# Kernel optimization log

Measured on AMD Instinct MI355X. Metric: run time of the kernel, lower is better.

The kernel has to match this reference:

```python
import jax, jax.numpy as jnp
import numpy as np

B, T = 1024, 39
NUM_C, NUM_STU, NUM_E, EMB = 123, 100000, 50000, 256
H = 123
IN1 = NUM_C + EMB  # 379


def setup_inputs() -> dict:
    key = jax.random.key(0)
    ks = jax.random.split(key, 32)
    f = lambda k, shp, s: jax.random.normal(k, shp, dtype=jnp.float32) * s
    inp = {}
    inp["q_maritx"] = jax.random.uniform(ks[0], (B, T, NUM_C), dtype=jnp.float32)
    inp["q_maritx_next"] = jax.random.uniform(ks[1], (B, T, NUM_C), dtype=jnp.float32)
    inp["concept"] = jax.random.randint(ks[2], (B, T), 0, NUM_C + 1)
    inp["s_id"] = jax.random.randint(ks[3], (B, 1), 0, NUM_STU + 1)
    inp["e_id"] = jax.random.randint(ks[4], (B, T), 0, NUM_E + 1)
    inp["r"] = jax.random.randint(ks[5], (B, T), 0, 2)
    inp["q_next"] = jax.random.randint(ks[6], (B, T), 0, NUM_E + 1)
    inp["concept_next"] = jax.random.randint(ks[7], (B, T), 0, NUM_C + 1)
    # learned parameters
    inp["emb_problem"] = f(ks[8], (NUM_E + 1, EMB), 1.0)
    inp["student_W"] = f(ks[9], (NUM_STU + 1, NUM_C), 1.0)
    inp["k_diff_W"] = f(ks[10], (NUM_E + 1, NUM_C), 1.0)
    inp["e_disc_W"] = f(ks[11], (NUM_E + 1, 1), 1.0)
    inp["answer_W"] = f(ks[12], (2, EMB), 1.0)
    inp["zz_W"] = f(ks[13], (NUM_C, NUM_C), 0.05)
    inp["zz_b"] = jnp.zeros((NUM_C,), jnp.float32)
    inp["d_t"] = f(ks[14], (1,), 1.0)
    inp["d_e"] = f(ks[15], (1,), 1.0)
    inp["W_ih"] = f(ks[16], (H, IN1), 0.05)
    inp["b_ih"] = jnp.zeros((H,), jnp.float32)
    inp["W_hh"] = f(ks[17], (H, H), 0.05)
    inp["b_hh"] = jnp.zeros((H,), jnp.float32)
    inp["W_tg"] = f(ks[18], (H, 1), 0.05)
    inp["b_tg"] = jnp.zeros((H,), jnp.float32)
    inp["W_z"] = f(ks[19], (H, IN1 + H), 0.05)
    inp["b_z"] = jnp.zeros((H,), jnp.float32)
    inp["W_h"] = f(ks[20], (H, IN1 + H), 0.05)
    inp["b_h"] = jnp.zeros((H,), jnp.float32)
    inp["p1_W"] = f(ks[21], (256, 502), 0.05)
    inp["p1_b"] = jnp.zeros((256,), jnp.float32)
    inp["p2_W"] = f(ks[22], (123, 256), 0.05)
    inp["p2_b"] = jnp.zeros((123,), jnp.float32)
    inp["p3_W"] = f(ks[23], (1, 123), 0.05)
    inp["p3_b"] = jnp.zeros((1,), jnp.float32)
    return inp


def _forward(q_maritx, q_maritx_next, emb_problem, student_W, k_diff_W, e_disc_W,
             answer_W, zz_W, zz_b, d_t, d_e, W_ih, b_ih, W_hh, b_hh, W_tg, b_tg,
             W_z, b_z, W_h, b_h, p1_W, p1_b, p2_W, p2_b, p3_W, p3_b,
             s_id, e_id, r, q_next):
    Bc, Tc = e_id.shape
    e_next_emb = emb_problem[q_next]                       # [B,T,256]
    s_prof = jax.nn.sigmoid(student_W[s_id])               # [B,1,123] (broadcasts vs repeat(1,39,1))
    k_diff = jax.nn.sigmoid(k_diff_W[e_id])                # [B,T,123]
    e_disc = jax.nn.sigmoid(e_disc_W[e_id]) * d_e          # [B,T,1]
    r_emb = answer_W[r]                                    # [B,T,256]
    concept_ab = jnp.einsum('btk,hk->bth', q_maritx, zz_W) + zz_b  # [B,T,123]
    x1 = jnp.concatenate([concept_ab * s_prof, r_emb], axis=-1)    # [B,T,379]
    # --- time-gated RNN: h_t = tanh(W_ih x_t + W_hh h + b) * sigmoid(tg(t)) ---
    Xp = jnp.einsum('bti,hi->bth', x1, W_ih) + b_ih
    tvec = jnp.arange(Tc, dtype=Xp.dtype)[:, None]
    gates = jax.nn.sigmoid(tvec * W_tg[:, 0][None, :] + b_tg)      # [T,123]
    h0 = jnp.zeros((Bc, W_hh.shape[0]), Xp.dtype)

    def step1(h, xs):
        xp, g = xs
        h = jnp.tanh(xp + h @ W_hh.T + b_hh) * g
        return h, h

    _, ys1 = jax.lax.scan(step1, h0, (Xp.transpose(1, 0, 2), gates))
    out_zz = ys1.transpose(1, 0, 2)                        # [B,T,123]
    # --- GRU-like cell (W_r unused in original forward) ---
    input_x1 = e_disc * (d_t * s_prof + (1.0 - d_t) * out_zz - k_diff) * q_maritx
    x2 = jnp.concatenate([input_x1, r_emb], axis=-1)       # [B,T,379]
    nin = x2.shape[-1]
    Wz_x, Wz_h = W_z[:, :nin], W_z[:, nin:]
    Wh_x, Wh_h = W_h[:, :nin], W_h[:, nin:]
    Zx = jnp.einsum('bti,hi->bth', x2, Wz_x) + b_z
    Hx = jnp.einsum('bti,hi->bth', x2, Wh_x) + b_h

    def step2(h, xs):
        zx, hx = xs
        z = jax.nn.sigmoid(zx + h @ Wz_h.T)
        ht = jnp.tanh(hx + h @ Wh_h.T)
        h = (1.0 - z) * h + z * ht
        return h, h

    _, ys2 = jax.lax.scan(step2, h0, (Zx.transpose(1, 0, 2), Hx.transpose(1, 0, 2)))
    outputs = ys2.transpose(1, 0, 2)                       # [B,T,123]
    hcat = jnp.concatenate([outputs, e_next_emb, q_maritx_next], axis=-1)  # [B,T,502]
    o1 = jax.nn.sigmoid(hcat @ p1_W.T + p1_b)  # dropout as identity (deterministic reference)
    o2 = jax.nn.sigmoid(o1 @ p2_W.T + p2_b)
    return jax.nn.sigmoid(o2 @ p3_W.T + p3_b)              # [B,T,1]


def reference(q_maritx, q_maritx_next, emb_problem, student_W, k_diff_W, e_disc_W,
              answer_W, zz_W, zz_b, d_t, d_e, W_ih, b_ih, W_hh, b_hh, W_tg, b_tg,
              W_z, b_z, W_h, b_h, p1_W, p1_b, p2_W, p2_b, p3_W, p3_b,
              concept, s_id, e_id, r, q_next, concept_next):
    # concept / concept_next embeddings are computed but unused in the original output
    return _forward(q_maritx, q_maritx_next, emb_problem, student_W, k_diff_W,
                    e_disc_W, answer_W, zz_W, zz_b, d_t, d_e, W_ih, b_ih, W_hh,
                    b_hh, W_tg, b_tg, W_z, b_z, W_h, b_h, p1_W, p1_b, p2_W,
                    p2_b, p3_W, p3_b, s_id, e_id, r, q_next)
```

## Files before the change

### kernel.cpp

```cpp
#include <hip/hip_runtime.h>
#include <hip/hip_bf16.h>

#define NRB 39936
#define BB 1024
#define TT 39
#define CC 123
#define EMBD 256
#define PCH 136

typedef __attribute__((ext_vector_type(8))) short short8;
typedef __attribute__((ext_vector_type(4))) short shortv4;
typedef __attribute__((ext_vector_type(4))) float floatx4;
typedef unsigned short us;

__device__ __forceinline__ float rcp_(float x){ return __builtin_amdgcn_rcpf(x); }
__device__ __forceinline__ float fsig(float x){ return rcp_(1.f + __expf(-x)); }
__device__ __forceinline__ float ftanh(float x){
  float ax = __builtin_fabsf(x);
  float e = __expf(-2.f*ax);
  float r = (1.f - e) * rcp_(1.f + e);
  return __builtin_copysignf(r, x);
}
__device__ __forceinline__ us f2bf(float x){
  union { float f; unsigned u; } v; v.f = x;
  unsigned r = v.u + 0x7FFFu + ((v.u >> 16) & 1u);
  return (us)(r >> 16);
}
__device__ __forceinline__ us f2bfh(float x){
  __bf16 h = (__bf16)x;
  return __builtin_bit_cast(us, h);
}
__device__ __forceinline__ float bf2f(us u){
  union { unsigned u; float f; } v; v.u = ((unsigned)u) << 16; return v.f;
}

__device__ __forceinline__ void lds_barrier(){
  __builtin_amdgcn_sched_barrier(0);
  asm volatile("s_waitcnt lgkmcnt(0)" ::: "memory");
  __builtin_amdgcn_s_barrier();
  __builtin_amdgcn_sched_barrier(0);
}

__device__ __forceinline__ void gl_lds16(void* lds, const void* g){
  __builtin_amdgcn_global_load_lds(
      (const __attribute__((address_space(1))) unsigned int*)g,
      (__attribute__((address_space(3))) unsigned int*)lds, 16, 0, 0);
}

#define G_RC 6
#define G_CW 1088
#define G_CAST 2496
#define G_HCAT 1872
#define G_PRE (G_RC + G_CW + G_CAST + G_HCAT)

__global__ __launch_bounds__(256) void k_pre(
    const float* __restrict__ W_ih, const float* __restrict__ W_z,
    const float* __restrict__ W_h, const float* __restrict__ answer_W,
    const float* __restrict__ zz_W, const float* __restrict__ W_hh,
    const float* __restrict__ p1_W, const float* __restrict__ p2_W,
    const float* __restrict__ emb, const int* __restrict__ q_next,
    const float* __restrict__ qmn, const float* __restrict__ q_m,
    float* __restrict__ rtab, us* __restrict__ wts,
    us* __restrict__ p1bf, us* __restrict__ p2bf,
    us* __restrict__ qbf, us* __restrict__ Abf)
{
  const int blk = blockIdx.x, tid = threadIdx.x;
  if (blk < G_RC){
    int which = blk >> 1, j = blk & 1, h = tid;
    if (h >= CC) return;
    const float* W; int stride;
    if (which==0){ W=W_ih; stride=379; } else if (which==1){ W=W_z; stride=502; } else { W=W_h; stride=502; }
    const float* a = answer_W + j*EMBD;
    const float* w = W + (size_t)h*stride + CC;
    float acc = 0.f;
    #pragma unroll 8
    for (int i=0;i<EMBD;i++) acc += w[i]*a[i];
    rtab[(which*2+j)*128 + h] = acc;
    return;
  }
  if (blk < G_RC + G_CW){
    int i = (blk - G_RC)*256 + tid;
    if (i < 7*16384){
      int w = i >> 14, idx = i & 16383, n = idx >> 7, k = idx & 127;
      float v = 0.f;
      if (n < CC && k < CC){
        if      (w==0) v = zz_W[n*CC + k];
        else if (w==1) v = W_ih[n*379 + k];
        else if (w==2) v = W_z [n*502 + k];
        else if (w==3) v = W_h [n*502 + k];
        else if (w==4) v = W_hh[n*CC + k];
        else if (w==5) v = W_z [n*502 + 379 + k];
        else           v = W_h [n*502 + 379 + k];
      }
      wts[i] = f2bf(v);
      return;
    }
    int j = i - 7*16384;
    if (j < 256*512){
      int n = j >> 9, k = j & 511;
      float v;
      if      (k < 379) v = p1_W[n*502 + k + 123];
      else if (k < 384) v = 0.f;
      else if (k < 507) v = p1_W[n*502 + (k - 384)];
      else              v = 0.f;
      p1bf[j] = f2bf(v);
      return;
    }
    j -= 256*512;
    if (j < 128*256){
      int n = j >> 8, k = j & 255;
      p2bf[j] = f2bf(n < CC ? p2_W[n*256 + k] : 0.f);
    }
    return;
  }
  if (blk < G_RC + G_CW + G_CAST){
    const size_t total = (size_t)NRB*128;
    for (size_t i = (size_t)(blk - G_RC - G_CW)*256 + tid; i < total; i += (size_t)G_CAST*256){
      int col = (int)(i & 127); size_t rp = i >> 7;
      int t = (int)(rp >> 10), b = (int)(rp & 1023);
      float v = (col < CC) ? q_m[((size_t)b*TT + t)*CC + col] : 0.f;
      qbf[i] = f2bf(v);
    }
    return;
  }
  {
    const size_t nchunk = (size_t)NRB*48;
    for (size_t c = (size_t)(blk - G_RC - G_CW - G_CAST)*256 + tid; c < nchunk; c += (size_t)G_HCAT*256){
      size_t row = c / 48;
      int c0 = (int)(c - row*48) * 8;
      short8 o;
      if (c0 < 256){
        int qn = q_next[row];
        float4 v0 = *(const float4*)(emb + (size_t)qn*EMBD + c0);
        float4 v1 = *(const float4*)(emb + (size_t)qn*EMBD + c0 + 4);
        o[0]=f2bf(v0.x); o[1]=f2bf(v0.y); o[2]=f2bf(v0.z); o[3]=f2bf(v0.w);
        o[4]=f2bf(v1.x); o[5]=f2bf(v1.y); o[6]=f2bf(v1.z); o[7]=f2bf(v1.w);
      } else {
        int j0 = c0 - 256;
        #pragma unroll
        for (int jj=0;jj<8;jj++){
          int j = j0 + jj;
          o[jj] = (j < CC) ? f2bf(qmn[row*CC + j]) : (short)0;
        }
      }
      *(short8*)(Abf + row*512 + c0) = o;
    }
  }
}

__global__ __launch_bounds__(256) void k_zz_elem(
    const us* __restrict__ X, const us* __restrict__ W,
    const float* __restrict__ zz_b,
    const float* __restrict__ q_m, const int* __restrict__ s_id,
    const int* __restrict__ e_id, const float* __restrict__ student_W,
    const float* __restrict__ k_diff_W, const float* __restrict__ e_disc_W,
    const float* __restrict__ d_t_p, const float* __restrict__ d_e_p,
    us* __restrict__ x1a, us* __restrict__ pre2, us* __restrict__ cqb)
{
  __shared__ __align__(16) us Asl[16][64][8];
  const int tid = threadIdx.x, w = tid >> 6, l = tid & 63, q = l >> 4, r16 = l & 15;
  const int rTile = blockIdx.x*64;
  short8 bfr[2][4];
  #pragma unroll
  for (int nt=0;nt<2;nt++){
    int n = w*32 + nt*16 + r16;
    #pragma unroll
    for (int kt=0;kt<4;kt++)
      bfr[nt][kt] = *(const short8*)(W + (size_t)n*128 + kt*32 + q*8);
  }
  #pragma unroll
  for (int i=0;i<4;i++){
    int seg = i*4 + w;
    gl_lds16(&Asl[seg][l][0], X + (size_t)(rTile+l)*128 + seg*8);
  }
  floatx4 acc[4][2];
  #pragma unroll
  for (int mt=0;mt<4;mt++){
    #pragma unroll
    for (int nt=0;nt<2;nt++){ acc[mt][nt][0]=0.f; acc[mt][nt][1]=0.f; acc[mt][nt][2]=0.f; acc[mt][nt][3]=0.f; }
  }
  __syncthreads();
  #pragma unroll
  for (int kt=0;kt<4;kt++){
    short8 af[4];
    #pragma unroll
    for (int mt=0;mt<4;mt++) af[mt] = *(const short8*)&Asl[kt*4+q][mt*16+r16][0];
    #pragma unroll
    for (int mt=0;mt<4;mt++){
      #pragma unroll
      for (int nt=0;nt<2;nt++)
        acc[mt][nt] = __builtin_amdgcn_mfma_f32_16x16x32_bf16(af[mt], bfr[nt][kt], acc[mt][nt], 0,0,0);
    }
  }
  const float dt = d_t_p[0], de = d_e_p[0];
  float zzb[2]; int colv[2];
  #pragma unroll
  for (int nt=0;nt<2;nt++){
    int col = w*32 + nt*16 + r16; colv[nt] = col;
    zzb[nt] = (col < CC) ? zz_b[col] : 0.f;
  }
  const int t = rTile >> 10;
  #pragma unroll
  for (int mt=0;mt<4;mt++){
    #pragma unroll
    for (int i=0;i<4;i++){
      int row = rTile + mt*16 + q*4 + i;
      int b = row & 1023;
      int g = b*TT + t;
      int btile = b >> 4, r = b & 15;
      int sid = s_id[b];
      int e   = e_id[g];
      float ed = fsig(e_disc_W[e]) * de;
      size_t base = ((size_t)t*64 + btile)*2048;
      #pragma unroll
      for (int nt=0;nt<2;nt++){
        int col = colv[nt];
        float x1v = 0.f, p2v = 0.f, cqv = 0.f;
        if (col < CC){
          float ab = acc[mt][nt][i] + zzb[nt];
          float sp = fsig(student_W[(size_t)sid*CC + col]);
          float kd = fsig(k_diff_W[(size_t)e*CC + col]);
          float qv = q_m[(size_t)g*CC + col];
          x1v = ab*sp;
          p2v = ed*(dt*sp - kd)*qv;
          cqv = ed*(1.f - dt)*qv;
        }
        x1a[base + (size_t)(((col>>5)*64 + ((col>>3)&3)*16 + r)*8) + (col&7)] = f2bf(x1v);
        size_t off = base + (size_t)(((col>>5)*64 + ((r>>2))*16 + (col&15))*8) + ((col>>4)&1)*4 + (r&3);
        pre2[off] = f2bf(p2v);
        cqb[off]  = f2bf(cqv);
      }
    }
  }
}

__global__ __launch_bounds__(512,1) void k_mid(
    const us* __restrict__ x1a, const us* __restrict__ pre2, const us* __restrict__ cqb,
    const us* __restrict__ Wih, const us* __restrict__ Whh,
    const us* __restrict__ Wzx, const us* __restrict__ Whx,
    const us* __restrict__ Wzh, const us* __restrict__ Whh2,
    const float* __restrict__ b_ih, const float* __restrict__ b_z, const float* __restrict__ b_h,
    const float* __restrict__ W_tg, const float* __restrict__ b_tg,
    const float* __restrict__ rtab, const int* __restrict__ r_idx,
    us* __restrict__ Abf)
{
  __shared__ __align__(16) us h1s[2][16*PCH];
  __shared__ __align__(16) us x2s[2][16*PCH];
  __shared__ __align__(16) us h2s[2][16*PCH];
  __shared__ int rint[TT*16];
  const int tid = threadIdx.x, w = tid >> 6, l = tid & 63, q = l >> 4, r16 = l & 15;
  const int bbase = blockIdx.x*16;
  const int n = w*16 + r16;

  short8 fih[4], fhh[4], fzx[4], fhx[4], fzh[4], fh2w[4];
  #pragma unroll
  for (int kt=0;kt<4;kt++){
    size_t wofs = (size_t)n*128 + kt*32 + q*8;
    fih[kt]  = *(const short8*)(Wih  + wofs);
    fhh[kt]  = *(const short8*)(Whh  + wofs);
    fzx[kt]  = *(const short8*)(Wzx  + wofs);
    fhx[kt]  = *(const short8*)(Whx  + wofs);
    fzh[kt]  = *(const short8*)(Wzh  + wofs);
    fh2w[kt] = *(const short8*)(Whh2 + wofs);
  }
  const bool vc = n < CC;
  const float bih = vc? b_ih[n]:0.f, bzv = vc? b_z[n]:0.f, bhv = vc? b_h[n]:0.f;
  const float wg = vc? W_tg[n]:0.f, bg = vc? b_tg[n]:0.f;
  const float r10 = vc? rtab[n]:0.f,     r11 = vc? rtab[128+n]:0.f;
  const float r20 = vc? rtab[256+n]:0.f, r21 = vc? rtab[384+n]:0.f;
  const float r30 = vc? rtab[512+n]:0.f, r31 = vc? rtab[640+n]:0.f;

  for (int i = tid; i < TT*16; i += 512)
    rint[i] = r_idx[(size_t)(bbase + (i & 15))*TT + (i >> 4)];
  for (int i = tid; i < 16*PCH; i += 512){ h1s[1][i] = 0; h2s[1][i] = 0; }

  short8 x1c[4];
  shortv4 pc4, cc4;
  {
    size_t base = (size_t)blockIdx.x*2048;
    #pragma unroll
    for (int kt=0;kt<4;kt++)
      x1c[kt] = *(const short8*)(x1a + base + (size_t)(kt*64 + q*16 + r16)*8);
    size_t cofs = base + (size_t)((w>>1)*64 + q*16 + r16)*8 + (size_t)(w&1)*4;
    pc4 = *(const shortv4*)(pre2 + cofs);
    cc4 = *(const shortv4*)(cqb + cofs);
  }
  __syncthreads();

  floatx4 accx;
  #pragma unroll
  for (int i=0;i<4;i++){ int rs = rint[q*4 + i]; accx[i] = bih + (rs ? r11 : r10); }
  #pragma unroll
  for (int kt=0;kt<4;kt++)
    accx = __builtin_amdgcn_mfma_f32_16x16x32_bf16(x1c[kt], fih[kt], accx, 0,0,0);

  floatx4 hold; hold[0]=0.f; hold[1]=0.f; hold[2]=0.f; hold[3]=0.f;

  for (int t=0; t<TT; t++){
    const int pA = t & 1, pO = pA ^ 1;
    short8 x1n[4]; shortv4 pcn, ccn;
    if (t < TT-1){
      size_t base = ((size_t)(t+1)*64 + blockIdx.x)*2048;
      #pragma unroll
      for (int kt=0;kt<4;kt++)
        x1n[kt] = *(const short8*)(x1a + base + (size_t)(kt*64 + q*16 + r16)*8);
      size_t cofs = base + (size_t)((w>>1)*64 + q*16 + r16)*8 + (size_t)(w&1)*4;
      pcn = *(const shortv4*)(pre2 + cofs);
      ccn = *(const shortv4*)(cqb + cofs);
    }
    short8 fr1[4];
    #pragma unroll
    for (int kt=0;kt<4;kt++)
      fr1[kt] = *(const short8*)&h1s[pO][r16*PCH + kt*32 + q*8];
    floatx4 acc1 = accx;
    #pragma unroll
    for (int kt=0;kt<4;kt++)
      acc1 = __builtin_amdgcn_mfma_f32_16x16x32_bf16(fr1[kt], fhh[kt], acc1, 0,0,0);
    float g = fsig((float)t*wg + bg);
    #pragma unroll
    for (int i=0;i<4;i++){
      float h1v = ftanh(acc1[i]) * g;
      h1s[pA][(q*4+i)*PCH + n] = f2bfh(h1v);
      float xv = bf2f((us)pc4[i]) + bf2f((us)cc4[i])*h1v;
      x2s[pA][(q*4+i)*PCH + n] = f2bfh(xv);
    }
    lds_barrier();
    if (t >= 1 && tid < 256){
      int row = tid >> 4, cs = tid & 15;
      short8 hv8 = *(const short8*)&h2s[pO][row*PCH + cs*8];
      *(short8*)(Abf + ((size_t)(bbase + row)*TT + (t-1))*512 + 384 + cs*8) = hv8;
    }
    short8 fx[4], fh[4];
    #pragma unroll
    for (int kt=0;kt<4;kt++){
      fx[kt] = *(const short8*)&x2s[pA][r16*PCH + kt*32 + q*8];
      fh[kt] = *(const short8*)&h2s[pO][r16*PCH + kt*32 + q*8];
    }
    floatx4 az, ahh;
    #pragma unroll
    for (int i=0;i<4;i++){
      int rs = rint[t*16 + q*4 + i];
      az[i]  = bzv + (rs ? r21 : r20);
      ahh[i] = bhv + (rs ? r31 : r30);
    }
    #pragma unroll
    for (int kt=0;kt<4;kt++){
      az  = __builtin_amdgcn_mfma_f32_16x16x32_bf16(fx[kt], fzx[kt], az, 0,0,0);
      az  = __builtin_amdgcn_mfma_f32_16x16x32_bf16(fh[kt], fzh[kt], az, 0,0,0);
      ahh = __builtin_amdgcn_mfma_f32_16x16x32_bf16(fx[kt], fhx[kt], ahh, 0,0,0);
      ahh = __builtin_amdgcn_mfma_f32_16x16x32_bf16(fh[kt], fh2w[kt], ahh, 0,0,0);
    }
    #pragma unroll
    for (int i=0;i<4;i++){
      float z  = fsig(az[i]);
      float th = ftanh(ahh[i]);
      hold[i] += z*(th - hold[i]);
      h2s[pA][(q*4+i)*PCH + n] = f2bfh(hold[i]);
    }
    if (t < TT-1){
      #pragma unroll
      for (int i=0;i<4;i++){ int rs = rint[(t+1)*16 + q*4 + i]; accx[i] = bih + (rs ? r11 : r10); }
      #pragma unroll
      for (int kt=0;kt<4;kt++)
        accx = __builtin_amdgcn_mfma_f32_16x16x32_bf16(x1n[kt], fih[kt], accx, 0,0,0);
      pc4 = pcn; cc4 = ccn;
    }
  }
  __syncthreads();
  if (tid < 256){
    int row = tid >> 4, cs = tid & 15;
    short8 hv8 = *(const short8*)&h2s[(TT-1)&1][row*PCH + cs*8];
    *(short8*)(Abf + ((size_t)(bbase + row)*TT + (TT-1))*512 + 384 + cs*8) = hv8;
  }
}

__global__ __launch_bounds__(256) void k_out(
    const us* __restrict__ Abf, const us* __restrict__ p1bf,
    const float* __restrict__ p1_b, const us* __restrict__ p2bf,
    const float* __restrict__ p2_b, const float* __restrict__ p3_W,
    const float* __restrict__ p3_b, float* __restrict__ out)
{
  __shared__ __align__(16) us smem[20480];
  __shared__ float red[64][4];
  us* Asl = smem;
  us* Bsl = smem + 4096;
  us* o1s = smem;
  const int tid = threadIdx.x;
  const int w = tid >> 6, l = tid & 63;
  const int q = l >> 4, r16 = l & 15;
  const int rTile = blockIdx.x * 64;
  floatx4 acc[4][4];
  #pragma unroll
  for (int a=0;a<4;a++){
    #pragma unroll
    for (int b=0;b<4;b++){ acc[a][b][0]=0.f; acc[a][b][1]=0.f; acc[a][b][2]=0.f; acc[a][b][3]=0.f; }
  }
  for (int c = 0; c < 8; c++){
    const int k0 = c*64;
    #pragma unroll
    for (int i=0;i<2;i++){
      int u = i*256 + tid; int seg = u>>6, m = u&63;
      gl_lds16(&Asl[(seg*64 + m)*8], Abf + (size_t)(rTile+m)*512 + k0 + seg*8);
    }
    #pragma unroll
    for (int i=0;i<8;i++){
      int u = i*256 + tid; int seg = u>>8, nn = u&255;
      gl_lds16(&Bsl[(seg*256 + nn)*8], p1bf + (size_t)nn*512 + k0 + seg*8);
    }
    __syncthreads();
    #pragma unroll
    for (int ks=0; ks<2; ks++){
      int seg = ks*4 + q;
      short8 af[4], bfr[4];
      #pragma unroll
      for (int mt=0;mt<4;mt++) af[mt] = *(const short8*)&Asl[(seg*64 + mt*16 + r16)*8];
      #pragma unroll
      for (int nt=0;nt<4;nt++) bfr[nt] = *(const short8*)&Bsl[(seg*256 + w*64 + nt*16 + r16)*8];
      #pragma unroll
      for (int mt=0;mt<4;mt++){
        #pragma unroll
        for (int nt=0;nt<4;nt++)
          acc[mt][nt] = __builtin_amdgcn_mfma_f32_16x16x32_bf16(af[mt], bfr[nt], acc[mt][nt], 0,0,0);
      }
    }
    __syncthreads();
  }
  #pragma unroll
  for (int nt=0;nt<4;nt++){
    int col = w*64 + nt*16 + r16;
    float bb = p1_b[col];
    #pragma unroll
    for (int mt=0;mt<4;mt++){
      #pragma unroll
      for (int i=0;i<4;i++)
        o1s[(mt*16 + q*4 + i)*264 + col] = f2bf(fsig(acc[mt][nt][i] + bb));
    }
  }
  __syncthreads();
  short8 bf2[2][8];
  #pragma unroll
  for (int nt=0;nt<2;nt++){
    int n2 = w*32 + nt*16 + r16;
    #pragma unroll
    for (int kt=0;kt<8;kt++)
      bf2[nt][kt] = *(const short8*)(p2bf + (size_t)n2*256 + kt*32 + q*8);
  }
  floatx4 ac2[4][2];
  #pragma unroll
  for (int mt=0;mt<4;mt++){
    #pragma unroll
    for (int nt=0;nt<2;nt++){ ac2[mt][nt][0]=0.f; ac2[mt][nt][1]=0.f; ac2[mt][nt][2]=0.f; ac2[mt][nt][3]=0.f; }
  }
  #pragma unroll
  for (int kt=0;kt<8;kt++){
    short8 af[4];
    #pragma unroll
    for (int mt=0;mt<4;mt++) af[mt] = *(const short8*)&o1s[(mt*16 + r16)*264 + kt*32 + q*8];
    #pragma unroll
    for (int mt=0;mt<4;mt++){
      #pragma unroll
      for (int nt=0;nt<2;nt++)
        ac2[mt][nt] = __builtin_amdgcn_mfma_f32_16x16x32_bf16(af[mt], bf2[nt][kt], ac2[mt][nt], 0,0,0);
    }
  }
  const int n0 = w*32 + r16, n1 = n0 + 16;
  const float pb0 = (n0<CC)? p2_b[n0]:0.f, pb1 = (n1<CC)? p2_b[n1]:0.f;
  const float p30 = (n0<CC)? p3_W[n0]:0.f, p31 = (n1<CC)? p3_W[n1]:0.f;
  #pragma unroll
  for (int mt=0;mt<4;mt++){
    #pragma unroll
    for (int i=0;i<4;i++){
      float s = fsig(ac2[mt][0][i]+pb0)*p30 + fsig(ac2[mt][1][i]+pb1)*p31;
      s += __shfl_xor(s,1,16); s += __shfl_xor(s,2,16);
      s += __shfl_xor(s,4,16); s += __shfl_xor(s,8,16);
      if (r16==0) red[mt*16 + q*4 + i][w] = s;
    }
  }
  __syncthreads();
  if (tid < 64){
    float o = red[tid][0]+red[tid][1]+red[tid][2]+red[tid][3] + p3_b[0];
    out[rTile + tid] = fsig(o);
  }
}

extern "C" void kernel_launch(void* const* d_in, const int* in_sizes, int n_in,
                              void* d_out, int out_size, void* d_ws, size_t ws_size,
                              hipStream_t stream) {
  const float* q_m       = (const float*)d_in[0];
  const float* q_m_next  = (const float*)d_in[1];
  const int*   s_id      = (const int*)d_in[3];
  const int*   e_id      = (const int*)d_in[4];
  const int*   r_idx     = (const int*)d_in[5];
  const int*   q_next    = (const int*)d_in[6];
  const float* emb_problem = (const float*)d_in[8];
  const float* student_W = (const float*)d_in[9];
  const float* k_diff_W  = (const float*)d_in[10];
  const float* e_disc_W  = (const float*)d_in[11];
  const float* answer_W  = (const float*)d_in[12];
  const float* zz_W      = (const float*)d_in[13];
  const float* zz_b      = (const float*)d_in[14];
  const float* d_t       = (const float*)d_in[15];
  const float* d_e       = (const float*)d_in[16];
  const float* W_ih      = (const float*)d_in[17];
  const float* b_ih      = (const float*)d_in[18];
  const float* W_hh      = (const float*)d_in[19];
  const float* W_tg      = (const float*)d_in[21];
  const float* b_tg      = (const float*)d_in[22];
  const float* W_z       = (const float*)d_in[23];
  const float* b_z       = (const float*)d_in[24];
  const float* W_h       = (const float*)d_in[25];
  const float* b_h       = (const float*)d_in[26];
  const float* p1_W      = (const float*)d_in[27];
  const float* p1_b      = (const float*)d_in[28];
  const float* p2_W      = (const float*)d_in[29];
  const float* p2_b      = (const float*)d_in[30];
  const float* p3_W      = (const float*)d_in[31];
  const float* p3_b      = (const float*)d_in[32];

  float* ws   = (float*)d_ws;
  float* rtab = ws;
  us* qbf  = (us*)(ws + 1024);
  us* x1a  = qbf  + (size_t)NRB*128;
  us* pre2 = x1a  + (size_t)NRB*128;
  us* cqb  = pre2 + (size_t)NRB*128;
  us* Abf  = cqb  + (size_t)NRB*128;
  us* wts  = Abf  + (size_t)NRB*512;
  us* p1bf = wts  + 7*16384;
  us* p2bf = p1bf + 256*512;

  const us* zzWbf  = wts + 0*16384;
  const us* Wih123 = wts + 1*16384;
  const us* Wz123  = wts + 2*16384;
  const us* Wh123  = wts + 3*16384;
  const us* Whhbf  = wts + 4*16384;
  const us* Wzhbf  = wts + 5*16384;
  const us* Whh2bf = wts + 6*16384;

  hipLaunchKernelGGL(k_pre, dim3(G_PRE), dim3(256), 0, stream,
                     W_ih, W_z, W_h, answer_W, zz_W, W_hh, p1_W, p2_W,
                     emb_problem, q_next, q_m_next, q_m,
                     rtab, wts, p1bf, p2bf, qbf, Abf);
  hipLaunchKernelGGL(k_zz_elem, dim3(NRB/64), dim3(256), 0, stream,
                     qbf, zzWbf, zz_b, q_m, s_id, e_id, student_W, k_diff_W,
                     e_disc_W, d_t, d_e, x1a, pre2, cqb);
  hipLaunchKernelGGL(k_mid, dim3(BB/16), dim3(512), 0, stream,
                     x1a, pre2, cqb, Wih123, Whhbf, Wz123, Wh123, Wzhbf, Whh2bf,
                     b_ih, b_z, b_h, W_tg, b_tg, rtab, r_idx, Abf);
  hipLaunchKernelGGL(k_out, dim3(NRB/64), dim3(256), 0, stream,
                     Abf, p1bf, p1_b, p2bf, p2_b, p3_W, p3_b, (float*)d_out);
}
```

Baseline: 376.2 us.

## Split recurrent kernel into two wave groups pipelining RNN1 and RNN2 stages

The k_mid recurrence is restructured so waves 0-3 compute the first RNN (ih/hh) for step k while waves 4-7 compute the second GRU-like RNN for step k-1, with each wave covering two 16-column tiles. This software-pipelines the two dependent stages across wave groups, leaving one barrier per step instead of a serial chain per step. Bias and r-table terms are pre-summed, and a large unused LDS pad is added that appears meant to limit occupancy. The risk is imbalance, since group B does twice the MFMA work of group A, plus an extra pipeline step.

```diff
diff --git a/kernel.cpp b/kernel.cpp
--- a/kernel.cpp
+++ b/kernel.cpp
@@ -32,13 +32,6 @@
 }
 __device__ __forceinline__ float bf2f(us u){
   union { unsigned u; float f; } v; v.u = ((unsigned)u) << 16; return v.f;
-}
-
-__device__ __forceinline__ void lds_barrier(){
-  __builtin_amdgcn_sched_barrier(0);
-  asm volatile("s_waitcnt lgkmcnt(0)" ::: "memory");
-  __builtin_amdgcn_s_barrier();
-  __builtin_amdgcn_sched_barrier(0);
 }
 
 __device__ __forceinline__ void gl_lds16(void* lds, const void* g){
@@ -248,125 +241,196 @@
   __shared__ __align__(16) us x2s[2][16*PCH];
   __shared__ __align__(16) us h2s[2][16*PCH];
   __shared__ int rint[TT*16];
-  const int tid = threadIdx.x, w = tid >> 6, l = tid & 63, q = l >> 4, r16 = l & 15;
+  __shared__ __align__(16) us lds_pad[27680];
+
+  const int tid = threadIdx.x, wid = tid >> 6, l = tid & 63, q = l >> 4, r16 = l & 15;
+  const bool isA = wid < 4;
+  const int gw = wid & 3;
   const int bbase = blockIdx.x*16;
-  const int n = w*16 + r16;
-
-  short8 fih[4], fhh[4], fzx[4], fhx[4], fzh[4], fh2w[4];
-  #pragma unroll
-  for (int kt=0;kt<4;kt++){
-    size_t wofs = (size_t)n*128 + kt*32 + q*8;
-    fih[kt]  = *(const short8*)(Wih  + wofs);
-    fhh[kt]  = *(const short8*)(Whh  + wofs);
-    fzx[kt]  = *(const short8*)(Wzx  + wofs);
-    fhx[kt]  = *(const short8*)(Whx  + wofs);
-    fzh[kt]  = *(const short8*)(Wzh  + wofs);
-    fh2w[kt] = *(const short8*)(Whh2 + wofs);
-  }
-  const bool vc = n < CC;
-  const float bih = vc? b_ih[n]:0.f, bzv = vc? b_z[n]:0.f, bhv = vc? b_h[n]:0.f;
-  const float wg = vc? W_tg[n]:0.f, bg = vc? b_tg[n]:0.f;
-  const float r10 = vc? rtab[n]:0.f,     r11 = vc? rtab[128+n]:0.f;
-  const float r20 = vc? rtab[256+n]:0.f, r21 = vc? rtab[384+n]:0.f;
-  const float r30 = vc? rtab[512+n]:0.f, r31 = vc? rtab[640+n]:0.f;
+  const int n0 = gw*32 + r16, n1 = n0 + 16;
+  if (Abf == (us*)0) lds_pad[tid] = (us)tid;
+
+  short8 w[4][2][4];
+  if (isA){
+    #pragma unroll
+    for (int tt=0;tt<2;tt++){
+      const int nn = n0 + tt*16;
+      #pragma unroll
+      for (int kt=0;kt<4;kt++){
+        size_t wofs = (size_t)nn*128 + kt*32 + q*8;
+        w[0][tt][kt] = *(const short8*)(Wih + wofs);
+        w[1][tt][kt] = *(const short8*)(Whh + wofs);
+      }
+    }
+  } else {
+    #pragma unroll
+    for (int tt=0;tt<2;tt++){
+      const int nn = n0 + tt*16;
+      #pragma unroll
+      for (int kt=0;kt<4;kt++){
+        size_t wofs = (size_t)nn*128 + kt*32 + q*8;
+        w[0][tt][kt] = *(const short8*)(Wzx + wofs);
+        w[1][tt][kt] = *(const short8*)(Wzh + wofs);
+        w[2][tt][kt] = *(const short8*)(Whx + wofs);
+        w[3][tt][kt] = *(const short8*)(Whh2 + wofs);
+      }
+    }
+  }
+
+  const bool v0 = n0 < CC, v1 = n1 < CC;
+  float ia0[2], ia1[2], ib0[2], ib1[2];
+  float wg0=0.f, bg0=0.f, wg1=0.f, bg1=0.f;
+  if (isA){
+    ia0[0] = v0 ? b_ih[n0] + rtab[n0]     : 0.f;
+    ia1[0] = v0 ? b_ih[n0] + rtab[128+n0] : 0.f;
+    ia0[1] = v1 ? b_ih[n1] + rtab[n1]     : 0.f;
+    ia1[1] = v1 ? b_ih[n1] + rtab[128+n1] : 0.f;
+    ib0[0]=0.f; ib1[0]=0.f; ib0[1]=0.f; ib1[1]=0.f;
+    wg0 = v0 ? W_tg[n0]:0.f; bg0 = v0 ? b_tg[n0]:0.f;
+    wg1 = v1 ? W_tg[n1]:0.f; bg1 = v1 ? b_tg[n1]:0.f;
+  } else {
+    ia0[0] = v0 ? b_z[n0] + rtab[256+n0] : 0.f;
+    ia1[0] = v0 ? b_z[n0] + rtab[384+n0] : 0.f;
+    ia0[1] = v1 ? b_z[n1] + rtab[256+n1] : 0.f;
+    ia1[1] = v1 ? b_z[n1] + rtab[384+n1] : 0.f;
+    ib0[0] = v0 ? b_h[n0] + rtab[512+n0] : 0.f;
+    ib1[0] = v0 ? b_h[n0] + rtab[640+n0] : 0.f;
+    ib0[1] = v1 ? b_h[n1] + rtab[512+n1] : 0.f;
+    ib1[1] = v1 ? b_h[n1] + rtab[640+n1] : 0.f;
+  }
 
   for (int i = tid; i < TT*16; i += 512)
     rint[i] = r_idx[(size_t)(bbase + (i & 15))*TT + (i >> 4)];
   for (int i = tid; i < 16*PCH; i += 512){ h1s[1][i] = 0; h2s[1][i] = 0; }
 
-  short8 x1c[4];
-  shortv4 pc4, cc4;
-  {
+  short8 x1c[4]; short8 pc8, cc8;
+  if (isA){
     size_t base = (size_t)blockIdx.x*2048;
     #pragma unroll
     for (int kt=0;kt<4;kt++)
       x1c[kt] = *(const short8*)(x1a + base + (size_t)(kt*64 + q*16 + r16)*8);
-    size_t cofs = base + (size_t)((w>>1)*64 + q*16 + r16)*8 + (size_t)(w&1)*4;
-    pc4 = *(const shortv4*)(pre2 + cofs);
-    cc4 = *(const shortv4*)(cqb + cofs);
+    size_t cofs = base + (size_t)(gw*64 + q*16 + r16)*8;
+    pc8 = *(const short8*)(pre2 + cofs);
+    cc8 = *(const short8*)(cqb + cofs);
   }
   __syncthreads();
 
-  floatx4 accx;
-  #pragma unroll
-  for (int i=0;i<4;i++){ int rs = rint[q*4 + i]; accx[i] = bih + (rs ? r11 : r10); }
-  #pragma unroll
-  for (int kt=0;kt<4;kt++)
-    accx = __builtin_amdgcn_mfma_f32_16x16x32_bf16(x1c[kt], fih[kt], accx, 0,0,0);
-
-  floatx4 hold; hold[0]=0.f; hold[1]=0.f; hold[2]=0.f; hold[3]=0.f;
-
-  for (int t=0; t<TT; t++){
-    const int pA = t & 1, pO = pA ^ 1;
-    short8 x1n[4]; shortv4 pcn, ccn;
-    if (t < TT-1){
-      size_t base = ((size_t)(t+1)*64 + blockIdx.x)*2048;
-      #pragma unroll
-      for (int kt=0;kt<4;kt++)
-        x1n[kt] = *(const short8*)(x1a + base + (size_t)(kt*64 + q*16 + r16)*8);
-      size_t cofs = base + (size_t)((w>>1)*64 + q*16 + r16)*8 + (size_t)(w&1)*4;
-      pcn = *(const shortv4*)(pre2 + cofs);
-      ccn = *(const shortv4*)(cqb + cofs);
-    }
-    short8 fr1[4];
-    #pragma unroll
-    for (int kt=0;kt<4;kt++)
-      fr1[kt] = *(const short8*)&h1s[pO][r16*PCH + kt*32 + q*8];
-    floatx4 acc1 = accx;
-    #pragma unroll
-    for (int kt=0;kt<4;kt++)
-      acc1 = __builtin_amdgcn_mfma_f32_16x16x32_bf16(fr1[kt], fhh[kt], acc1, 0,0,0);
-    float g = fsig((float)t*wg + bg);
-    #pragma unroll
-    for (int i=0;i<4;i++){
-      float h1v = ftanh(acc1[i]) * g;
-      h1s[pA][(q*4+i)*PCH + n] = f2bfh(h1v);
-      float xv = bf2f((us)pc4[i]) + bf2f((us)cc4[i])*h1v;
-      x2s[pA][(q*4+i)*PCH + n] = f2bfh(xv);
-    }
-    lds_barrier();
-    if (t >= 1 && tid < 256){
-      int row = tid >> 4, cs = tid & 15;
-      short8 hv8 = *(const short8*)&h2s[pO][row*PCH + cs*8];
-      *(short8*)(Abf + ((size_t)(bbase + row)*TT + (t-1))*512 + 384 + cs*8) = hv8;
-    }
-    short8 fx[4], fh[4];
+  floatx4 accx0, accx1;
+  if (isA){
+    int4 rs = *(const int4*)&rint[q*4];
+    accx0[0] = rs.x ? ia1[0] : ia0[0];  accx1[0] = rs.x ? ia1[1] : ia0[1];
+    accx0[1] = rs.y ? ia1[0] : ia0[0];  accx1[1] = rs.y ? ia1[1] : ia0[1];
+    accx0[2] = rs.z ? ia1[0] : ia0[0];  accx1[2] = rs.z ? ia1[1] : ia0[1];
+    accx0[3] = rs.w ? ia1[0] : ia0[0];  accx1[3] = rs.w ? ia1[1] : ia0[1];
     #pragma unroll
     for (int kt=0;kt<4;kt++){
-      fx[kt] = *(const short8*)&x2s[pA][r16*PCH + kt*32 + q*8];
-      fh[kt] = *(const short8*)&h2s[pO][r16*PCH + kt*32 + q*8];
-    }
-    floatx4 az, ahh;
-    #pragma unroll
-    for (int i=0;i<4;i++){
-      int rs = rint[t*16 + q*4 + i];
-      az[i]  = bzv + (rs ? r21 : r20);
-      ahh[i] = bhv + (rs ? r31 : r30);
-    }
-    #pragma unroll
-    for (int kt=0;kt<4;kt++){
-      az  = __builtin_amdgcn_mfma_f32_16x16x32_bf16(fx[kt], fzx[kt], az, 0,0,0);
-      az  = __builtin_amdgcn_mfma_f32_16x16x32_bf16(fh[kt], fzh[kt], az, 0,0,0);
-      ahh = __builtin_amdgcn_mfma_f32_16x16x32_bf16(fx[kt], fhx[kt], ahh, 0,0,0);
-      ahh = __builtin_amdgcn_mfma_f32_16x16x32_bf16(fh[kt], fh2w[kt], ahh, 0,0,0);
-    }
-    #pragma unroll
-    for (int i=0;i<4;i++){
-      float z  = fsig(az[i]);
-      float th = ftanh(ahh[i]);
-      hold[i] += z*(th - hold[i]);
-      h2s[pA][(q*4+i)*PCH + n] = f2bfh(hold[i]);
-    }
-    if (t < TT-1){
-      #pragma unroll
-      for (int i=0;i<4;i++){ int rs = rint[(t+1)*16 + q*4 + i]; accx[i] = bih + (rs ? r11 : r10); }
-      #pragma unroll
-      for (int kt=0;kt<4;kt++)
-        accx = __builtin_amdgcn_mfma_f32_16x16x32_bf16(x1n[kt], fih[kt], accx, 0,0,0);
-      pc4 = pcn; cc4 = ccn;
-    }
-  }
-  __syncthreads();
+      accx0 = __builtin_amdgcn_mfma_f32_16x16x32_bf16(x1c[kt], w[0][0][kt], accx0, 0,0,0);
+      accx1 = __builtin_amdgcn_mfma_f32_16x16x32_bf16(x1c[kt], w[0][1][kt], accx1, 0,0,0);
+    }
+  }
+  floatx4 hold0, hold1;
+  hold0[0]=0.f; hold0[1]=0.f; hold0[2]=0.f; hold0[3]=0.f;
+  hold1[0]=0.f; hold1[1]=0.f; hold1[2]=0.f; hold1[3]=0.f;
+
+  for (int k=0; k<=TT; ++k){
+    const int pA = k & 1;
+    if (isA){
+      short8 x1n[4]; short8 pcn, ccn;
+      if (k+1 < TT){
+        size_t base = ((size_t)(k+1)*64 + blockIdx.x)*2048;
+        #pragma unroll
+        for (int kt=0;kt<4;kt++)
+          x1n[kt] = *(const short8*)(x1a + base + (size_t)(kt*64 + q*16 + r16)*8);
+        size_t cofs = base + (size_t)(gw*64 + q*16 + r16)*8;
+        pcn = *(const short8*)(pre2 + cofs);
+        ccn = *(const short8*)(cqb + cofs);
+      }
+      if (k < TT){
+        short8 fr1[4];
+        #pragma unroll
+        for (int kt=0;kt<4;kt++)
+          fr1[kt] = *(const short8*)&h1s[pA^1][r16*PCH + kt*32 + q*8];
+        floatx4 a0 = accx0, a1 = accx1;
+        #pragma unroll
+        for (int kt=0;kt<4;kt++){
+          a0 = __builtin_amdgcn_mfma_f32_16x16x32_bf16(fr1[kt], w[1][0][kt], a0, 0,0,0);
+          a1 = __builtin_amdgcn_mfma_f32_16x16x32_bf16(fr1[kt], w[1][1][kt], a1, 0,0,0);
+        }
+        float g0 = fsig((float)k*wg0 + bg0);
+        float g1 = fsig((float)k*wg1 + bg1);
+        #pragma unroll
+        for (int i=0;i<4;i++){
+          float h1v0 = ftanh(a0[i]) * g0;
+          h1s[pA][(q*4+i)*PCH + n0] = f2bfh(h1v0);
+          float xv0 = bf2f((us)pc8[i]) + bf2f((us)cc8[i])*h1v0;
+          x2s[pA][(q*4+i)*PCH + n0] = f2bfh(xv0);
+          float h1v1 = ftanh(a1[i]) * g1;
+          h1s[pA][(q*4+i)*PCH + n1] = f2bfh(h1v1);
+          float xv1 = bf2f((us)pc8[4+i]) + bf2f((us)cc8[4+i])*h1v1;
+          x2s[pA][(q*4+i)*PCH + n1] = f2bfh(xv1);
+        }
+      }
+      if (k >= 2){
+        int row = tid >> 4, cs = tid & 15;
+        short8 hv8 = *(const short8*)&h2s[pA][row*PCH + cs*8];
+        *(short8*)(Abf + ((size_t)(bbase + row)*TT + (k-2))*512 + 384 + cs*8) = hv8;
+      }
+      if (k+1 < TT){
+        int4 rs = *(const int4*)&rint[(k+1)*16 + q*4];
+        accx0[0] = rs.x ? ia1[0] : ia0[0];  accx1[0] = rs.x ? ia1[1] : ia0[1];
+        accx0[1] = rs.y ? ia1[0] : ia0[0];  accx1[1] = rs.y ? ia1[1] : ia0[1];
+        accx0[2] = rs.z ? ia1[0] : ia0[0];  accx1[2] = rs.z ? ia1[1] : ia0[1];
+        accx0[3] = rs.w ? ia1[0] : ia0[0];  accx1[3] = rs.w ? ia1[1] : ia0[1];
+        #pragma unroll
+        for (int kt=0;kt<4;kt++){
+          accx0 = __builtin_amdgcn_mfma_f32_16x16x32_bf16(x1n[kt], w[0][0][kt], accx0, 0,0,0);
+          accx1 = __builtin_amdgcn_mfma_f32_16x16x32_bf16(x1n[kt], w[0][1][kt], accx1, 0,0,0);
+        }
+        pc8 = pcn; cc8 = ccn;
+      }
+    } else if (k >= 1){
+      const int t = k-1, pB = t & 1;
+      short8 fx[4], fh[4];
+      #pragma unroll
+      for (int kt=0;kt<4;kt++){
+        fx[kt] = *(const short8*)&x2s[pB][r16*PCH + kt*32 + q*8];
+        fh[kt] = *(const short8*)&h2s[pB^1][r16*PCH + kt*32 + q*8];
+      }
+      int4 rs = *(const int4*)&rint[t*16 + q*4];
+      floatx4 az0, az1, ah0, ah1;
+      az0[0] = rs.x ? ia1[0] : ia0[0];  ah0[0] = rs.x ? ib1[0] : ib0[0];
+      az0[1] = rs.y ? ia1[0] : ia0[0];  ah0[1] = rs.y ? ib1[0] : ib0[0];
+      az0[2] = rs.z ? ia1[0] : ia0[0];  ah0[2] = rs.z ? ib1[0] : ib0[0];
+      az0[3] = rs.w ? ia1[0] : ia0[0];  ah0[3] = rs.w ? ib1[0] : ib0[0];
+      az1[0] = rs.x ? ia1[1] : ia0[1];  ah1[0] = rs.x ? ib1[1] : ib0[1];
+      az1[1] = rs.y ? ia1[1] : ia0[1];  ah1[1] = rs.y ? ib1[1] : ib0[1];
+      az1[2] = rs.z ? ia1[1] : ia0[1];  ah1[2] = rs.z ? ib1[1] : ib0[1];
+      az1[3] = rs.w ? ia1[1] : ia0[1];  ah1[3] = rs.w ? ib1[1] : ib0[1];
+      #pragma unroll
+      for (int kt=0;kt<4;kt++){
+        az0 = __builtin_amdgcn_mfma_f32_16x16x32_bf16(fx[kt], w[0][0][kt], az0, 0,0,0);
+        az0 = __builtin_amdgcn_mfma_f32_16x16x32_bf16(fh[kt], w[1][0][kt], az0, 0,0,0);
+        ah0 = __builtin_amdgcn_mfma_f32_16x16x32_bf16(fx[kt], w[2][0][kt], ah0, 0,0,0);
+        ah0 = __builtin_amdgcn_mfma_f32_16x16x32_bf16(fh[kt], w[3][0][kt], ah0, 0,0,0);
+        az1 = __builtin_amdgcn_mfma_f32_16x16x32_bf16(fx[kt], w[0][1][kt], az1, 0,0,0);
+        az1 = __builtin_amdgcn_mfma_f32_16x16x32_bf16(fh[kt], w[1][1][kt], az1, 0,0,0);
+        ah1 = __builtin_amdgcn_mfma_f32_16x16x32_bf16(fx[kt], w[2][1][kt], ah1, 0,0,0);
+        ah1 = __builtin_amdgcn_mfma_f32_16x16x32_bf16(fh[kt], w[3][1][kt], ah1, 0,0,0);
+      }
+      #pragma unroll
+      for (int i=0;i<4;i++){
+        float z0  = fsig(az0[i]);
+        float th0 = ftanh(ah0[i]);
+        hold0[i] += z0*(th0 - hold0[i]);
+        h2s[pB][(q*4+i)*PCH + n0] = f2bfh(hold0[i]);
+        float z1  = fsig(az1[i]);
+        float th1 = ftanh(ah1[i]);
+        hold1[i] += z1*(th1 - hold1[i]);
+        h2s[pB][(q*4+i)*PCH + n1] = f2bfh(hold1[i]);
+      }
+    }
+    __syncthreads();
+  }
   if (tid < 256){
     int row = tid >> 4, cs = tid & 15;
     short8 hv8 = *(const short8*)&h2s[(TT-1)&1][row*PCH + cs*8];
```

Result: no change. 370.9 us (-1.4%).
